# Performance work log

Measured on AMD Instinct MI355X. Metric: run time of the kernel, lower is better.

The kernel has to match this reference:

```python
import jax, jax.numpy as jnp
import numpy as np

B, S, HQ, HKV, D = 2, 2048, 32, 8, 128
ROPE_BASE = 10000.0
NEG_INF = -1e9


def setup_inputs() -> dict:
    key = jax.random.key(0)
    kq, kk, kv = jax.random.split(key, 3)
    q = jax.random.normal(kq, (B, S, HQ, D), dtype=jnp.float32)
    k = jax.random.normal(kk, (B, S, HKV, D), dtype=jnp.float32)
    v = jax.random.normal(kv, (B, S, HKV, D), dtype=jnp.float32)
    # Llama rotary tables: [S, D] with freqs duplicated across the two halves
    inv_freq = 1.0 / (ROPE_BASE ** (jnp.arange(0, D, 2, dtype=jnp.float32) / D))
    freqs = jnp.arange(S, dtype=jnp.float32)[:, None] * inv_freq[None, :]  # [S, D/2]
    emb = jnp.concatenate([freqs, freqs], axis=-1)  # [S, D]
    cos = jnp.cos(emb)
    sin = jnp.sin(emb)
    # causal additive mask [B, 1, S, S]: 0 on/below diagonal, -1e9 above
    causal = jnp.tril(jnp.ones((S, S), dtype=bool))
    attention_mask = jnp.where(causal, 0.0, NEG_INF).astype(jnp.float32)
    attention_mask = jnp.broadcast_to(attention_mask[None, None], (B, 1, S, S))
    return {
        "query_states": q,
        "key_states": k,
        "value_states": v,
        "cos": cos,
        "sin": sin,
        "attention_mask": attention_mask,
        "softmax_scale": float(1.0 / np.sqrt(D)),
    }


def _rotate_half(x):
    h = x.shape[-1] // 2
    return jnp.concatenate([-x[..., h:], x[..., :h]], axis=-1)


def _apply_rope(x, cos, sin):
    # x: [B, S, H, D]; cos/sin: [S, D] -> broadcast over batch and heads
    c = cos[None, :, None, :]
    s = sin[None, :, None, :]
    return x * c + _rotate_half(x) * s


def reference(query_states, key_states, value_states, cos, sin, attention_mask, softmax_scale):
    if attention_mask.ndim == 4 and attention_mask.shape[1] == 1:
        attention_mask = attention_mask[:, 0]  # [B, S, S]
    q = _apply_rope(query_states, cos, sin)          # [B, S, HQ, D]
    k = _apply_rope(key_states, cos, sin)            # [B, S, HKV, D]
    v = value_states                                  # [B, S, HKV, D]
    groups = q.shape[2] // k.shape[2]
    k = jnp.repeat(k, groups, axis=2)                 # [B, S, HQ, D]
    v = jnp.repeat(v, groups, axis=2)
    scores = jnp.einsum("bqhd,bkhd->bhqk", q, k) * softmax_scale
    scores = scores + attention_mask[:, None, :, :]   # broadcast over heads
    probs = jax.nn.softmax(scores, axis=-1)
    out = jnp.einsum("bhqk,bkhd->bqhd", probs, v)     # [B, S, HQ, D]
    return out
```

## Files before the change

kernel.cpp:

```cpp
#include <hip/hip_runtime.h>
#include <stdint.h>

typedef unsigned short u16;
typedef unsigned int   u32;
typedef short bf16x8 __attribute__((ext_vector_type(8)));
typedef u16   u16x8  __attribute__((ext_vector_type(8)));
typedef float f32x4  __attribute__((ext_vector_type(4)));

#define B_   2
#define S_   2048
#define HQ_  32
#define HKV_ 8
#define D_   128
#define SCALE 0.08838834764831845f

#define KR_ELEMS (B_*HKV_*S_*D_)

#define NK_T (B_*S_*HKV_*64)
#define NV_T (B_*HKV_*16*(S_/2))

__device__ __forceinline__ float b2f(u16 x) { return __uint_as_float(((u32)x) << 16); }
__device__ __forceinline__ u16 f2b(float f) {
  u32 u = __float_as_uint(f);
  return (u16)((u + 0x7FFFu + ((u >> 16) & 1u)) >> 16);
}
__device__ __forceinline__ bool is_f32(const void* cs) {
  return ((const u32*)cs)[0] == 0x3F800000u;
}

__device__ __forceinline__ void gload16(const u16* g, u16* l) {
  __builtin_amdgcn_global_load_lds(
      (const __attribute__((address_space(1))) u32*)g,
      (__attribute__((address_space(3))) u32*)l, 16, 0, 0);
}

__global__ __launch_bounds__(256) void rope_pre(
    const void* __restrict__ kin, const void* __restrict__ vin,
    const void* __restrict__ cs, const void* __restrict__ sn, u16* __restrict__ ws)
{
  const bool f32 = is_f32(cs);
  int tid = blockIdx.x * 256 + threadIdx.x;
  if (tid < NK_T) {
    int d2 = tid & 63;
    int s  = (tid >> 6) & (S_ - 1);
    int h  = (tid >> 17) & (HKV_ - 1);
    int b  = tid >> 20;
    int gi = ((b*S_ + s)*HKV_ + h)*D_ + d2;
    int ci = s*D_ + d2;
    float xa, xb, c, si;
    if (f32) {
      const float* kf = (const float*)kin;
      xa = kf[gi]; xb = kf[gi + 64];
      c  = ((const float*)cs)[ci]; si = ((const float*)sn)[ci];
    } else {
      const u16* kb = (const u16*)kin;
      xa = b2f(kb[gi]); xb = b2f(kb[gi + 64]);
      c  = b2f(((const u16*)cs)[ci]); si = b2f(((const u16*)sn)[ci]);
    }
    int oi = ((b*HKV_ + h)*S_ + s)*D_ + d2;
    ws[oi]      = f2b(xa*c - xb*si);
    ws[oi + 64] = f2b(xb*c + xa*si);
  } else {
    int t3   = tid - NK_T;
    int spLo = t3 & 15;
    int c4   = (t3 >> 4) & 15;
    int spHi = (t3 >> 8) & 63;
    int h    = (t3 >> 14) & (HKV_ - 1);
    int b    = t3 >> 17;
    int sp   = spHi*16 + spLo;
    int gi0  = ((b*S_ + 2*sp)*HKV_ + h)*D_ + 8*c4;
    u16 e0[8], e1[8];
    if (f32) {
      const float* vf = (const float*)vin;
      f32x4 a0 = *(const f32x4*)(vf + gi0);
      f32x4 a1 = *(const f32x4*)(vf + gi0 + 4);
      f32x4 b0 = *(const f32x4*)(vf + gi0 + HKV_*D_);
      f32x4 b1 = *(const f32x4*)(vf + gi0 + HKV_*D_ + 4);
#pragma unroll
      for (int j = 0; j < 4; ++j) {
        e0[j] = f2b(a0[j]); e0[4+j] = f2b(a1[j]);
        e1[j] = f2b(b0[j]); e1[4+j] = f2b(b1[j]);
      }
    } else {
      const u16* vb = (const u16*)vin;
      u16x8 v0 = *(const u16x8*)(vb + gi0);
      u16x8 v1 = *(const u16x8*)(vb + gi0 + HKV_*D_);
#pragma unroll
      for (int j = 0; j < 8; ++j) { e0[j] = v0[j]; e1[j] = v1[j]; }
    }
    u32* vtd = (u32*)(ws + KR_ELEMS);
    int rowbase = (b*HKV_ + h)*D_ + 8*c4;
#pragma unroll
    for (int j = 0; j < 8; ++j)
      vtd[(rowbase + j)*(S_/2) + sp] = (u32)e0[j] | ((u32)e1[j] << 16);
  }
}

__global__ __launch_bounds__(256, 4) void flash_attn(
    const void* __restrict__ qg, const void* __restrict__ cs, const void* __restrict__ sn,
    const u16* __restrict__ ws, float* __restrict__ out)
{
  __shared__ __attribute__((aligned(16))) u16 lds[10752];

  const bool f32 = is_f32(cs);
  const int t = threadIdx.x;
  const int lane = t & 63, w = t >> 6;
  const int lq = lane & 15, quad = lane >> 4;

  int bx = blockIdx.x;
  int g = bx & 7, ii = bx >> 3;
  int combo = g*2 + (ii >> 6);
  int b = combo >> 3, kvh = combo & 7;
  int rr = ii & 63;
  int h   = kvh*4 + (rr & 3);
  int qbp = rr >> 2;

  const u16* Kr = ws + (b*HKV_ + kvh)*S_*D_;
  const u16* Vt = ws + KR_ELEMS + (b*HKV_ + kvh)*D_*S_;

  for (int half = 0; half < 2; ++half) {
    int qb = half ? (31 - qbp) : qbp;
    int q0 = qb * 64;
    if (half) __syncthreads();

#pragma unroll
    for (int it = 0; it < 2; ++it) {
      int tp = it*256 + t;
      int row = tp >> 3, j = tp & 7;
      int qbase = ((b*S_ + q0 + row)*HQ_ + h)*D_ + 8*j;
      int cbase = (q0 + row)*D_ + 8*j;
      float a[8], bb[8], cc[8], ssv[8];
      if (f32) {
        const float* qf32 = (const float*)qg;
        f32x4 a0 = *(const f32x4*)(qf32 + qbase);
        f32x4 a1 = *(const f32x4*)(qf32 + qbase + 4);
        f32x4 b0 = *(const f32x4*)(qf32 + qbase + 64);
        f32x4 b1 = *(const f32x4*)(qf32 + qbase + 68);
        f32x4 c0 = *(const f32x4*)((const float*)cs + cbase);
        f32x4 c1 = *(const f32x4*)((const float*)cs + cbase + 4);
        f32x4 s0 = *(const f32x4*)((const float*)sn + cbase);
        f32x4 s1 = *(const f32x4*)((const float*)sn + cbase + 4);
#pragma unroll
        for (int e = 0; e < 4; ++e) {
          a[e] = a0[e];  a[4+e] = a1[e];  bb[e] = b0[e]; bb[4+e] = b1[e];
          cc[e] = c0[e]; cc[4+e] = c1[e]; ssv[e] = s0[e]; ssv[4+e] = s1[e];
        }
      } else {
        const u16* qb16 = (const u16*)qg;
        u16x8 xa = *(const u16x8*)(qb16 + qbase);
        u16x8 xb = *(const u16x8*)(qb16 + qbase + 64);
        u16x8 cv = *(const u16x8*)((const u16*)cs + cbase);
        u16x8 sv = *(const u16x8*)((const u16*)sn + cbase);
#pragma unroll
        for (int e = 0; e < 8; ++e) {
          a[e] = b2f(xa[e]); bb[e] = b2f(xb[e]);
          cc[e] = b2f(cv[e]); ssv[e] = b2f(sv[e]);
        }
      }
      u16 o0[8], o1[8];
#pragma unroll
      for (int e = 0; e < 8; ++e) {
        o0[e] = f2b(a[e]*cc[e] - bb[e]*ssv[e]);
        o1[e] = f2b(bb[e]*cc[e] + a[e]*ssv[e]);
      }
      int c0 = j >> 2, e0 = (j & 3) * 8;
      *(u16x8*)&lds[c0*2048 + row*32 + e0]       = *(u16x8*)o0;
      *(u16x8*)&lds[(c0 + 2)*2048 + row*32 + e0] = *(u16x8*)o1;
    }
    __syncthreads();
    bf16x8 qf[4];
#pragma unroll
    for (int c = 0; c < 4; ++c)
      qf[c] = *(const bf16x8*)&lds[c*2048 + (w*16 + lq)*32 + quad*8];

    f32x4 o[8];
#pragma unroll
    for (int dt = 0; dt < 8; ++dt) o[dt] = (f32x4){0.f, 0.f, 0.f, 0.f};
    float m_i = -1e30f, l_i = 0.f;
    const int qrow = q0 + w*16 + lq;

    const int nkb = 2*qb + 2;
    for (int kb = 0; kb < nkb; ++kb) {
      const int n0 = kb * 32;
      __syncthreads();
#pragma unroll
      for (int it = 0; it < 2; ++it) {
        int flat = (t + it*256) * 8;
        int c = flat >> 10, n = (flat >> 5) & 31, e = flat & 31;
        gload16(Kr + (n0 + n)*D_ + c*32 + e, &lds[flat]);
      }
#pragma unroll
      for (int it = 0; it < 2; ++it) {
        int flat = (t + it*256) * 8;
        int d = flat >> 5, n = flat & 31;
        gload16(Vt + d*S_ + n0 + n, &lds[4096 + flat]);
      }
      __syncthreads();

      f32x4 sc0 = {0,0,0,0}, sc1 = {0,0,0,0};
#pragma unroll
      for (int c = 0; c < 4; ++c) {
        bf16x8 k0 = *(const bf16x8*)&lds[c*1024 + lq*32 + quad*8];
        bf16x8 k1 = *(const bf16x8*)&lds[c*1024 + (16 + lq)*32 + quad*8];
        sc0 = __builtin_amdgcn_mfma_f32_16x16x32_bf16(k0, qf[c], sc0, 0, 0, 0);
        sc1 = __builtin_amdgcn_mfma_f32_16x16x32_bf16(k1, qf[c], sc1, 0, 0, 0);
      }

      const int kk = n0 + quad*4;
      float s0[4], s1[4];
#pragma unroll
      for (int r = 0; r < 4; ++r) {
        s0[r] = (kk + r      <= qrow) ? sc0[r]*SCALE : -1e30f;
        s1[r] = (kk + 16 + r <= qrow) ? sc1[r]*SCALE : -1e30f;
      }
      float mx = fmaxf(fmaxf(fmaxf(s0[0], s0[1]), fmaxf(s0[2], s0[3])),
                       fmaxf(fmaxf(s1[0], s1[1]), fmaxf(s1[2], s1[3])));
      mx = fmaxf(mx, __shfl_xor(mx, 16));
      mx = fmaxf(mx, __shfl_xor(mx, 32));
      float mn = fmaxf(m_i, mx);
      float al = __expf(m_i - mn);
      float p0[4], p1[4];
      float rs = 0.f;
#pragma unroll
      for (int r = 0; r < 4; ++r) {
        p0[r] = __expf(s0[r] - mn);
        p1[r] = __expf(s1[r] - mn);
        rs += p0[r] + p1[r];
      }
      rs += __shfl_xor(rs, 16);
      rs += __shfl_xor(rs, 32);
      l_i = l_i*al + rs;
      m_i = mn;
#pragma unroll
      for (int dt = 0; dt < 8; ++dt) {
#pragma unroll
        for (int r = 0; r < 4; ++r) o[dt][r] *= al;
      }

      u16* pw = &lds[8192 + w*640];
      u16 pk0[4], pk1[4];
#pragma unroll
      for (int r = 0; r < 4; ++r) { pk0[r] = f2b(p0[r]); pk1[r] = f2b(p1[r]); }
      *(uint64_t*)&pw[lq*40 + quad*4]      = *(uint64_t*)pk0;
      *(uint64_t*)&pw[lq*40 + 16 + quad*4] = *(uint64_t*)pk1;
      asm volatile("s_waitcnt lgkmcnt(0)" ::: "memory");
      bf16x8 pf = *(const bf16x8*)&pw[lq*40 + quad*8];

#pragma unroll
      for (int dt = 0; dt < 8; ++dt) {
        bf16x8 vf = *(const bf16x8*)&lds[4096 + (dt*16 + lq)*32 + quad*8];
        o[dt] = __builtin_amdgcn_mfma_f32_16x16x32_bf16(vf, pf, o[dt], 0, 0, 0);
      }
    }

    float inv = 1.0f / l_i;
    float* op = out + ((b*S_ + qrow)*HQ_ + h)*D_ + quad*4;
#pragma unroll
    for (int dt = 0; dt < 8; ++dt) {
      f32x4 v = { o[dt][0]*inv, o[dt][1]*inv, o[dt][2]*inv, o[dt][3]*inv };
      *(f32x4*)(op + dt*16) = v;
    }
  }
}

extern "C" void kernel_launch(void* const* d_in, const int* in_sizes, int n_in,
                              void* d_out, int out_size, void* d_ws, size_t ws_size,
                              hipStream_t stream) {
  const void* q  = d_in[0];
  const void* k  = d_in[1];
  const void* v  = d_in[2];
  const void* cs = d_in[3];
  const void* sn = d_in[4];
  u16*   ws  = (u16*)d_ws;
  float* out = (float*)d_out;

  const int npre = (NK_T + NV_T) / 256;
  rope_pre<<<npre, 256, 0, stream>>>(k, v, cs, sn, ws);
  flash_attn<<<B_*HQ_*(S_/128), 256, 0, stream>>>(q, cs, sn, ws, out);
}
```

Baseline: 296.2 us.

## Double-buffer K/V tiles, swizzle LDS, lazy softmax rescale, tiled V transpose

The attention kernel now prefetches the next K/V tile into a second LDS buffer while the current one is computed, and uses an XOR swizzle on LDS addresses to cut bank conflicts. The online softmax only rescales the accumulator when the running max grows by more than a threshold, which skips most rescale multiplies. The preprocessing kernel vectorizes the K RoPE work and transposes V through an LDS tile so that global writes are coalesced. These additions raise LDS use, which may lower occupancy, and the lazy rescale relies on exp headroom staying within fp32 range.

```diff
diff --git a/kernel.cpp b/kernel.cpp
--- a/kernel.cpp
+++ b/kernel.cpp
@@ -5,6 +5,7 @@
 typedef unsigned int   u32;
 typedef short bf16x8 __attribute__((ext_vector_type(8)));
 typedef u16   u16x8  __attribute__((ext_vector_type(8)));
+typedef u16   u16x4  __attribute__((ext_vector_type(4)));
 typedef float f32x4  __attribute__((ext_vector_type(4)));
 
 #define B_   2
@@ -16,8 +17,10 @@
 
 #define KR_ELEMS (B_*HKV_*S_*D_)
 
-#define NK_T (B_*S_*HKV_*64)
-#define NV_T (B_*HKV_*16*(S_/2))
+#define KT_BLOCKS ((B_*S_*HKV_*16) / 256)
+#define VT_BLOCKS (B_*HKV_*(S_/64))
+
+#define SWZ(x) ((x) ^ (((x) >> 3) & 0x70))
 
 __device__ __forceinline__ float b2f(u16 x) { return __uint_as_float(((u32)x) << 16); }
 __device__ __forceinline__ u16 f2b(float f) {
@@ -39,60 +42,98 @@
     const void* __restrict__ cs, const void* __restrict__ sn, u16* __restrict__ ws)
 {
   const bool f32 = is_f32(cs);
-  int tid = blockIdx.x * 256 + threadIdx.x;
-  if (tid < NK_T) {
-    int d2 = tid & 63;
-    int s  = (tid >> 6) & (S_ - 1);
-    int h  = (tid >> 17) & (HKV_ - 1);
-    int b  = tid >> 20;
-    int gi = ((b*S_ + s)*HKV_ + h)*D_ + d2;
-    int ci = s*D_ + d2;
-    float xa, xb, c, si;
+  const int bx = blockIdx.x;
+  const int t  = threadIdx.x;
+  __shared__ u16 tile[64 * 136];
+
+  if (bx < KT_BLOCKS) {
+    int tid = bx*256 + t;
+    int j4 = tid & 15;
+    int s  = (tid >> 4) & (S_ - 1);
+    int h  = (tid >> 15) & (HKV_ - 1);
+    int b  = tid >> 18;
+    int gi = ((b*S_ + s)*HKV_ + h)*D_ + 4*j4;
+    int ci = s*D_ + 4*j4;
+    float xa[4], xb[4], c[4], si[4];
     if (f32) {
       const float* kf = (const float*)kin;
-      xa = kf[gi]; xb = kf[gi + 64];
-      c  = ((const float*)cs)[ci]; si = ((const float*)sn)[ci];
+      f32x4 a0 = *(const f32x4*)(kf + gi);
+      f32x4 b0 = *(const f32x4*)(kf + gi + 64);
+      f32x4 c0 = *(const f32x4*)((const float*)cs + ci);
+      f32x4 s0 = *(const f32x4*)((const float*)sn + ci);
+#pragma unroll
+      for (int e = 0; e < 4; ++e) { xa[e]=a0[e]; xb[e]=b0[e]; c[e]=c0[e]; si[e]=s0[e]; }
     } else {
-      const u16* kb = (const u16*)kin;
-      xa = b2f(kb[gi]); xb = b2f(kb[gi + 64]);
-      c  = b2f(((const u16*)cs)[ci]); si = b2f(((const u16*)sn)[ci]);
-    }
-    int oi = ((b*HKV_ + h)*S_ + s)*D_ + d2;
-    ws[oi]      = f2b(xa*c - xb*si);
-    ws[oi + 64] = f2b(xb*c + xa*si);
+      const u16* kb16 = (const u16*)kin;
+      u16x4 a0 = *(const u16x4*)(kb16 + gi);
+      u16x4 b0 = *(const u16x4*)(kb16 + gi + 64);
+      u16x4 c0 = *(const u16x4*)((const u16*)cs + ci);
+      u16x4 s0 = *(const u16x4*)((const u16*)sn + ci);
+#pragma unroll
+      for (int e = 0; e < 4; ++e) { xa[e]=b2f(a0[e]); xb[e]=b2f(b0[e]); c[e]=b2f(c0[e]); si[e]=b2f(s0[e]); }
+    }
+    u16 o0[4], o1[4];
+#pragma unroll
+    for (int e = 0; e < 4; ++e) {
+      o0[e] = f2b(xa[e]*c[e] - xb[e]*si[e]);
+      o1[e] = f2b(xb[e]*c[e] + xa[e]*si[e]);
+    }
+    int oi = ((b*HKV_ + h)*S_ + s)*D_ + 4*j4;
+    *(u16x4*)(ws + oi)      = *(u16x4*)o0;
+    *(u16x4*)(ws + oi + 64) = *(u16x4*)o1;
   } else {
-    int t3   = tid - NK_T;
-    int spLo = t3 & 15;
-    int c4   = (t3 >> 4) & 15;
-    int spHi = (t3 >> 8) & 63;
-    int h    = (t3 >> 14) & (HKV_ - 1);
-    int b    = t3 >> 17;
-    int sp   = spHi*16 + spLo;
-    int gi0  = ((b*S_ + 2*sp)*HKV_ + h)*D_ + 8*c4;
-    u16 e0[8], e1[8];
-    if (f32) {
-      const float* vf = (const float*)vin;
-      f32x4 a0 = *(const f32x4*)(vf + gi0);
-      f32x4 a1 = *(const f32x4*)(vf + gi0 + 4);
-      f32x4 b0 = *(const f32x4*)(vf + gi0 + HKV_*D_);
-      f32x4 b1 = *(const f32x4*)(vf + gi0 + HKV_*D_ + 4);
-#pragma unroll
-      for (int j = 0; j < 4; ++j) {
-        e0[j] = f2b(a0[j]); e0[4+j] = f2b(a1[j]);
-        e1[j] = f2b(b0[j]); e1[4+j] = f2b(b1[j]);
-      }
-    } else {
-      const u16* vb = (const u16*)vin;
-      u16x8 v0 = *(const u16x8*)(vb + gi0);
-      u16x8 v1 = *(const u16x8*)(vb + gi0 + HKV_*D_);
-#pragma unroll
-      for (int j = 0; j < 8; ++j) { e0[j] = v0[j]; e1[j] = v1[j]; }
-    }
-    u32* vtd = (u32*)(ws + KR_ELEMS);
-    int rowbase = (b*HKV_ + h)*D_ + 8*c4;
-#pragma unroll
-    for (int j = 0; j < 8; ++j)
-      vtd[(rowbase + j)*(S_/2) + sp] = (u32)e0[j] | ((u32)e1[j] << 16);
+    int vb = bx - KT_BLOCKS;
+    int sb = vb & 31;
+    int h  = (vb >> 5) & (HKV_ - 1);
+    int b  = vb >> 8;
+    int s0 = sb * 64;
+#pragma unroll
+    for (int it = 0; it < 8; ++it) {
+      int task = it*256 + t;
+      int c4 = task & 31;
+      int r  = task >> 5;
+      int gi = ((b*S_ + s0 + r)*HKV_ + h)*D_ + 4*c4;
+      u16 e[4];
+      if (f32) {
+        f32x4 a = *(const f32x4*)((const float*)vin + gi);
+#pragma unroll
+        for (int j = 0; j < 4; ++j) e[j] = f2b(a[j]);
+      } else {
+        u16x4 a = *(const u16x4*)((const u16*)vin + gi);
+#pragma unroll
+        for (int j = 0; j < 4; ++j) e[j] = a[j];
+      }
+      *(u16x4*)&tile[r*136 + 4*c4] = *(u16x4*)e;
+    }
+    __syncthreads();
+    u32* vtd = (u32*)(ws + KR_ELEMS) + (b*HKV_ + h)*D_*(S_/2);
+#pragma unroll
+    for (int it = 0; it < 16; ++it) {
+      int task = it*256 + t;
+      int sp = task & 31, d = task >> 5;
+      u32 lo = tile[(2*sp)*136 + d];
+      u32 hi = tile[(2*sp + 1)*136 + d];
+      vtd[d*(S_/2) + s0/2 + sp] = lo | (hi << 16);
+    }
+  }
+}
+
+__device__ __forceinline__ void stage_tile(const u16* __restrict__ Kr,
+                                           const u16* __restrict__ Vt,
+                                           u16* lds, int bufbyte, int n0, int t) {
+#pragma unroll
+  for (int it = 0; it < 2; ++it) {
+    int a = (t + it*256) * 16;
+    int l = SWZ(a);
+    gload16(Kr + (n0 + ((l >> 6) & 31))*D_ + (l >> 11)*32 + ((l >> 4) & 3)*8,
+            (u16*)((char*)lds + bufbyte + a));
+  }
+#pragma unroll
+  for (int it = 0; it < 2; ++it) {
+    int a = (t + it*256) * 16;
+    int l = SWZ(a);
+    gload16(Vt + (l >> 6)*S_ + n0 + ((l >> 4) & 3)*8,
+            (u16*)((char*)lds + bufbyte + 8192 + a));
   }
 }
 
@@ -100,7 +141,7 @@
     const void* __restrict__ qg, const void* __restrict__ cs, const void* __restrict__ sn,
     const u16* __restrict__ ws, float* __restrict__ out)
 {
-  __shared__ __attribute__((aligned(16))) u16 lds[10752];
+  __shared__ __attribute__((aligned(16))) u16 lds[18944];
 
   const bool f32 = is_f32(cs);
   const int t = threadIdx.x;
@@ -163,45 +204,56 @@
         o0[e] = f2b(a[e]*cc[e] - bb[e]*ssv[e]);
         o1[e] = f2b(bb[e]*cc[e] + a[e]*ssv[e]);
       }
-      int c0 = j >> 2, e0 = (j & 3) * 8;
-      *(u16x8*)&lds[c0*2048 + row*32 + e0]       = *(u16x8*)o0;
-      *(u16x8*)&lds[(c0 + 2)*2048 + row*32 + e0] = *(u16x8*)o1;
+      int A0 = (j >> 2)*4096 + row*64 + (j & 3)*16;
+      int A1 = A0 + 8192;
+      *(u16x8*)((char*)lds + SWZ(A0)) = *(u16x8*)o0;
+      *(u16x8*)((char*)lds + SWZ(A1)) = *(u16x8*)o1;
     }
     __syncthreads();
     bf16x8 qf[4];
-#pragma unroll
-    for (int c = 0; c < 4; ++c)
-      qf[c] = *(const bf16x8*)&lds[c*2048 + (w*16 + lq)*32 + quad*8];
+    const int R = w*16 + lq;
+#pragma unroll
+    for (int c = 0; c < 4; ++c) {
+      int L = c*4096 + R*64 + quad*16;
+      qf[c] = *(const bf16x8*)((const char*)lds + SWZ(L));
+    }
+    asm volatile("s_waitcnt lgkmcnt(0)" ::: "memory");
+    __syncthreads();
 
     f32x4 o[8];
 #pragma unroll
     for (int dt = 0; dt < 8; ++dt) o[dt] = (f32x4){0.f, 0.f, 0.f, 0.f};
     float m_i = -1e30f, l_i = 0.f;
     const int qrow = q0 + w*16 + lq;
-
     const int nkb = 2*qb + 2;
+
+    stage_tile(Kr, Vt, lds, 0, 0, t);
+
     for (int kb = 0; kb < nkb; ++kb) {
+      const int cur = kb & 1;
+      asm volatile("" ::: "memory");
+      __builtin_amdgcn_s_barrier();
+      asm volatile("" ::: "memory");
+      if (kb + 1 < nkb) {
+        stage_tile(Kr, Vt, lds, (cur ^ 1)*16384, (kb + 1)*32, t);
+        asm volatile("s_waitcnt vmcnt(4)" ::: "memory");
+      } else {
+        asm volatile("s_waitcnt vmcnt(0)" ::: "memory");
+      }
+      __builtin_amdgcn_s_barrier();
+      asm volatile("" ::: "memory");
+
       const int n0 = kb * 32;
-      __syncthreads();
-#pragma unroll
-      for (int it = 0; it < 2; ++it) {
-        int flat = (t + it*256) * 8;
-        int c = flat >> 10, n = (flat >> 5) & 31, e = flat & 31;
-        gload16(Kr + (n0 + n)*D_ + c*32 + e, &lds[flat]);
-      }
-#pragma unroll
-      for (int it = 0; it < 2; ++it) {
-        int flat = (t + it*256) * 8;
-        int d = flat >> 5, n = flat & 31;
-        gload16(Vt + d*S_ + n0 + n, &lds[4096 + flat]);
-      }
-      __syncthreads();
+      const char* kbase = (const char*)lds + cur*16384;
+      const char* vbase = kbase + 8192;
 
       f32x4 sc0 = {0,0,0,0}, sc1 = {0,0,0,0};
 #pragma unroll
       for (int c = 0; c < 4; ++c) {
-        bf16x8 k0 = *(const bf16x8*)&lds[c*1024 + lq*32 + quad*8];
-        bf16x8 k1 = *(const bf16x8*)&lds[c*1024 + (16 + lq)*32 + quad*8];
+        int L0 = c*2048 + lq*64 + quad*16;
+        int L1 = L0 + 1024;
+        bf16x8 k0 = *(const bf16x8*)(kbase + SWZ(L0));
+        bf16x8 k1 = *(const bf16x8*)(kbase + SWZ(L1));
         sc0 = __builtin_amdgcn_mfma_f32_16x16x32_bf16(k0, qf[c], sc0, 0, 0, 0);
         sc1 = __builtin_amdgcn_mfma_f32_16x16x32_bf16(k1, qf[c], sc1, 0, 0, 0);
       }
@@ -217,27 +269,30 @@
                        fmaxf(fmaxf(s1[0], s1[1]), fmaxf(s1[2], s1[3])));
       mx = fmaxf(mx, __shfl_xor(mx, 16));
       mx = fmaxf(mx, __shfl_xor(mx, 32));
-      float mn = fmaxf(m_i, mx);
-      float al = __expf(m_i - mn);
+      if (!__all(mx - m_i <= 8.0f)) {
+        float mn = fmaxf(m_i, mx);
+        float al = __expf(m_i - mn);
+        l_i *= al;
+#pragma unroll
+        for (int dt = 0; dt < 8; ++dt) {
+#pragma unroll
+          for (int r = 0; r < 4; ++r) o[dt][r] *= al;
+        }
+        m_i = mn;
+      }
       float p0[4], p1[4];
       float rs = 0.f;
 #pragma unroll
       for (int r = 0; r < 4; ++r) {
-        p0[r] = __expf(s0[r] - mn);
-        p1[r] = __expf(s1[r] - mn);
+        p0[r] = __expf(s0[r] - m_i);
+        p1[r] = __expf(s1[r] - m_i);
         rs += p0[r] + p1[r];
       }
       rs += __shfl_xor(rs, 16);
       rs += __shfl_xor(rs, 32);
-      l_i = l_i*al + rs;
-      m_i = mn;
-#pragma unroll
-      for (int dt = 0; dt < 8; ++dt) {
-#pragma unroll
-        for (int r = 0; r < 4; ++r) o[dt][r] *= al;
-      }
-
-      u16* pw = &lds[8192 + w*640];
+      l_i += rs;
+
+      u16* pw = &lds[16384 + w*640];
       u16 pk0[4], pk1[4];
 #pragma unroll
       for (int r = 0; r < 4; ++r) { pk0[r] = f2b(p0[r]); pk1[r] = f2b(p1[r]); }
@@ -248,7 +303,8 @@
 
 #pragma unroll
       for (int dt = 0; dt < 8; ++dt) {
-        bf16x8 vf = *(const bf16x8*)&lds[4096 + (dt*16 + lq)*32 + quad*8];
+        int Lv = (dt*16 + lq)*64 + quad*16;
+        bf16x8 vf = *(const bf16x8*)(vbase + SWZ(Lv));
         o[dt] = __builtin_amdgcn_mfma_f32_16x16x32_bf16(vf, pf, o[dt], 0, 0, 0);
       }
     }
@@ -274,7 +330,6 @@
   u16*   ws  = (u16*)d_ws;
   float* out = (float*)d_out;
 
-  const int npre = (NK_T + NV_T) / 256;
-  rope_pre<<<npre, 256, 0, stream>>>(k, v, cs, sn, ws);
+  rope_pre<<<KT_BLOCKS + VT_BLOCKS, 256, 0, stream>>>(k, v, cs, sn, ws);
   flash_attn<<<B_*HQ_*(S_/128), 256, 0, stream>>>(q, cs, sn, ws, out);
 }
```

Result: faster. 283.2 us (-4.4%).
